# Kernel optimization log

Measured on AMD Instinct MI355X. Metric: run time of the kernel, lower is better.

The kernel has to match this reference:

```python
import jax, jax.numpy as jnp
import numpy as np
from jax import lax

N, M, T, V, C_IN, C_OUT, KT, PAD = 16, 2, 300, 25, 64, 64, 9, 4
BN_EPS = 1e-5

# NTU-RGB+D 25-joint skeleton edges (0-indexed), symmetric, plus self-loops
_NTU_EDGES = [(0,1),(1,20),(2,20),(3,2),(4,20),(5,4),(6,5),(7,6),(8,20),(9,8),
              (10,9),(11,10),(12,0),(13,12),(14,13),(15,14),(16,0),(17,16),
              (18,17),(19,18),(21,22),(22,7),(23,24),(24,11)]

def _build_adj():
    A = np.zeros((V, V), dtype=np.float32)
    for i, j in _NTU_EDGES:
        A[i, j] = 1.0
        A[j, i] = 1.0
    A += np.eye(V, dtype=np.float32)  # self-loops (DGL GCN preprocessing)
    return jnp.asarray(A)


def setup_inputs() -> dict:
    key = jax.random.key(0)
    ks = jax.random.split(key, 8)
    stdv = 1.0 / np.sqrt(C_OUT)
    # conv_init: normal(0, sqrt(2/(out_channels*prod(kernel))))
    conv_std = np.sqrt(2.0 / (C_OUT * KT * 1))
    return {
        "h": jax.random.normal(ks[0], (N * M * T * V, C_IN), dtype=jnp.float32),
        "adj": _build_adj(),
        "gcn_w": jax.random.uniform(ks[1], (C_IN, C_OUT), minval=-stdv, maxval=stdv, dtype=jnp.float32),
        "gcn_b": jax.random.uniform(ks[2], (C_OUT,), minval=-stdv, maxval=stdv, dtype=jnp.float32),
        "conv_w": conv_std * jax.random.normal(ks[3], (C_OUT, C_OUT, KT, 1), dtype=jnp.float32),
        "conv_b": jnp.zeros((C_OUT,), dtype=jnp.float32),
        "bn_gamma": jnp.ones((C_OUT,), dtype=jnp.float32),
        "bn_beta": jnp.zeros((C_OUT,), dtype=jnp.float32),
        "bn_mean": 0.1 * jax.random.normal(ks[4], (C_OUT,), dtype=jnp.float32),
        "bn_var": jax.random.uniform(ks[5], (C_OUT,), minval=0.5, maxval=1.5, dtype=jnp.float32),
    }


def reference(h, adj, gcn_w, gcn_b, conv_w, conv_b, bn_gamma, bn_beta, bn_mean, bn_var):
    # ---- GCNLayer (dropout is identity at eval) ----
    # symmetric norm = deg^{-1/2}, identical across the N*M*T copies of the skeleton
    norm = adj.sum(axis=1) ** -0.5                      # (V,)
    x = h @ gcn_w                                        # (N*M*T*V, C_OUT)
    x = x.reshape(-1, V, C_OUT) * norm[:, None]          # pre-norm scale
    x = jnp.einsum('vu,buc->bvc', adj, x)                # copy_src + sum aggregation
    x = x * norm[:, None] + gcn_b                        # post-norm scale + bias
    x = jax.nn.relu(x)

    # ---- TemporalConvNetwork ----
    v = x.reshape(N, M, T, V, C_OUT)
    v = v.transpose(0, 1, 4, 2, 3).reshape(N * M, C_OUT, T, V)   # (NM, C, T, V)
    v = lax.conv_general_dilated(v, conv_w, window_strides=(1, 1),
                                 padding=[(PAD, PAD), (0, 0)],
                                 dimension_numbers=('NCHW', 'OIHW', 'NCHW'))
    v = v + conv_b[None, :, None, None]
    inv_std = bn_gamma / jnp.sqrt(bn_var + BN_EPS)       # eval-mode BatchNorm2d
    v = (v - bn_mean[None, :, None, None]) * inv_std[None, :, None, None] + bn_beta[None, :, None, None]
    v = jax.nn.relu(v)
    v = v.reshape(N, M, C_OUT, T, V).transpose(0, 1, 3, 4, 2)    # (N, M, T, V, C)

    # ---- residual (downt is None since in_feats == out_feats and stride == 1) ----
    return v + h.reshape(N, M, T, V, C_IN)
```

## Files before the change

### kernel.cpp

```cpp
#include <hip/hip_runtime.h>
#include <hip/hip_bf16.h>


typedef __bf16 bf16x8 __attribute__((ext_vector_type(8)));
typedef __bf16 bf16x4 __attribute__((ext_vector_type(4)));
typedef float  f32x4  __attribute__((ext_vector_type(4)));

#define Y_OFF   0
#define WC2_OFF 30720000
#define WGT_OFF 30793728
#define A2P_OFF 30801920
#define SC_OFF  30803968
#define SH_OFF  30804224

__global__ __launch_bounds__(256) void prep_kernel(
    const float* __restrict__ adj, const float* __restrict__ gcn_w,
    const float* __restrict__ conv_w, const float* __restrict__ conv_b,
    const float* __restrict__ bn_g, const float* __restrict__ bn_b,
    const float* __restrict__ bn_m, const float* __restrict__ bn_v,
    __bf16* __restrict__ wc2, __bf16* __restrict__ wgt,
    __bf16* __restrict__ a2p, float* __restrict__ scale, float* __restrict__ shift) {
  int tid = threadIdx.x;
  for (int e = blockIdx.x * 256 + tid; e < 36864; e += gridDim.x * 256) {
    int j = e & 7, t1 = e >> 3, c = t1 & 63, g = t1 >> 6;
    int kap = g * 8 + j, kt = kap >> 6, ci = kap & 63;
    wc2[e] = (__bf16)conv_w[(c * 64 + ci) * 9 + kt];
  }
  if (blockIdx.x == 0) {
    for (int e = tid; e < 4096; e += 256) {
      int c = e >> 6, k = e & 63;
      wgt[e] = (__bf16)gcn_w[k * 64 + c];
    }
  } else if (blockIdx.x == 1) {
    for (int e = tid; e < 1024; e += 256) {
      int v = e >> 5, u = e & 31;
      float val = 0.f;
      if (v < 25 && u < 25) {
        float dv = 0.f, du = 0.f;
        for (int t = 0; t < 25; ++t) { dv += adj[v * 25 + t]; du += adj[u * 25 + t]; }
        val = rsqrtf(dv) * adj[v * 25 + u] * rsqrtf(du);
      }
      a2p[e] = (__bf16)val;
    }
  } else if (blockIdx.x == 2) {
    if (tid < 64) {
      float sc = bn_g[tid] * rsqrtf(bn_v[tid] + 1e-5f);
      scale[tid] = sc;
      shift[tid] = (conv_b[tid] - bn_m[tid]) * sc + bn_b[tid];
    }
  }
}

__global__ __launch_bounds__(64) void gcn_kernel(
    const float* __restrict__ h, const __bf16* __restrict__ wgt_g,
    const __bf16* __restrict__ a2p_g, const float* __restrict__ gcn_b,
    __bf16* __restrict__ y) {
  __shared__ __align__(16) __bf16 hb[2048];
  __shared__ __align__(16) __bf16 x1t[64 * 40];
  int lane = threadIdx.x;
  int l15 = lane & 15, quad = lane >> 4;
  int skel = blockIdx.x;
  int nm = skel / 300, tloc = skel - nm * 300;

  bf16x8 awg[4][2];
  for (int mt = 0; mt < 4; ++mt)
    for (int kk = 0; kk < 2; ++kk)
      awg[mt][kk] = *(const bf16x8*)&wgt_g[(mt * 16 + l15) * 64 + kk * 32 + quad * 8];
  bf16x8 ba[2];
  for (int nt = 0; nt < 2; ++nt)
    ba[nt] = *(const bf16x8*)&a2p_g[(nt * 16 + l15) * 32 + quad * 8];

  if (lane < 56) *(uint4*)&hb[1600 + lane * 8] = (uint4){0u, 0u, 0u, 0u};
  for (int it = 0; it < 7; ++it) {
    int u = it * 4 + quad;
    if (u < 25) {
      float4 hv = *(const float4*)&h[(skel * 25 + u) * 64 + l15 * 4];
      bf16x4 b4; b4[0] = (__bf16)hv.x; b4[1] = (__bf16)hv.y; b4[2] = (__bf16)hv.z; b4[3] = (__bf16)hv.w;
      int ch = l15 >> 1;
      *(bf16x4*)&hb[u * 64 + (((ch ^ (u & 7)) * 8) | ((l15 & 1) * 4))] = b4;
    }
  }
  for (int mt = 0; mt < 4; ++mt)
    for (int nt = 0; nt < 2; ++nt) {
      f32x4 acc = {0.f, 0.f, 0.f, 0.f};
      int u = nt * 16 + l15;
      for (int kk = 0; kk < 2; ++kk) {
        bf16x8 b = *(const bf16x8*)&hb[u * 64 + (((kk * 4 + quad) ^ (u & 7)) * 8)];
        acc = __builtin_amdgcn_mfma_f32_16x16x32_bf16(awg[mt][kk], b, acc, 0, 0, 0);
      }
      int c0 = mt * 16 + quad * 4;
      for (int r = 0; r < 4; ++r) x1t[(c0 + r) * 40 + u] = (__bf16)acc[r];
    }
  for (int mt = 0; mt < 4; ++mt)
    for (int nt = 0; nt < 2; ++nt) {
      f32x4 acc = {0.f, 0.f, 0.f, 0.f};
      bf16x8 a = *(const bf16x8*)&x1t[(mt * 16 + l15) * 40 + quad * 8];
      acc = __builtin_amdgcn_mfma_f32_16x16x32_bf16(a, ba[nt], acc, 0, 0, 0);
      int v = nt * 16 + l15, c0 = mt * 16 + quad * 4;
      if (v < 25) {
        float4 bias = *(const float4*)&gcn_b[c0];
        bf16x4 o;
        o[0] = (__bf16)fmaxf(acc[0] + bias.x, 0.f);
        o[1] = (__bf16)fmaxf(acc[1] + bias.y, 0.f);
        o[2] = (__bf16)fmaxf(acc[2] + bias.z, 0.f);
        o[3] = (__bf16)fmaxf(acc[3] + bias.w, 0.f);
        int ch = (c0 >> 3) ^ (v & 7);
        *(bf16x4*)&hb[v * 64 + ((ch * 8) | (c0 & 7))] = o;
      }
    }
  for (int e = lane; e < 200; e += 64) {
    int v = e >> 3, ch = e & 7;
    uint4 val = *(const uint4*)&hb[v * 64 + ((ch ^ (v & 7)) * 8)];
    *(uint4*)&y[((nm * 25 + v) * 300 + tloc) * 64 + ch * 8] = val;
  }
}

__global__ __launch_bounds__(256, 6) void conv_kernel(
    const __bf16* __restrict__ y, const __bf16* __restrict__ wc2,
    const float* __restrict__ scale, const float* __restrict__ shift,
    const float* __restrict__ h, float* __restrict__ out) {
  __shared__ __align__(16) __bf16 my[72 * 64];
  int tid = threadIdx.x, w = tid >> 6, lane = tid & 63;
  int l15 = lane & 15, quad = lane >> 4;
  int ti = blockIdx.x, vv = blockIdx.y, nm = blockIdx.z;
  int t0 = (ti < 4) ? ti * 64 : 236;

  {
    const __bf16* ybase = &y[((nm * 25 + vv) * 300) * 64];
    uint4 stg[3];
    for (int it = 0; it < 3; ++it) {
      int idx = it * 256 + tid;
      uint4 val = {0u, 0u, 0u, 0u};
      if (idx < 576) {
        int r = idx >> 3, ch = idx & 7, tg = t0 - 4 + r;
        if (tg >= 0 && tg < 300) val = *(const uint4*)&ybase[tg * 64 + ch * 8];
      }
      stg[it] = val;
    }
    for (int it = 0; it < 3; ++it) {
      int idx = it * 256 + tid;
      if (idx < 576) {
        int r = idx >> 3, ch = idx & 7;
        *(uint4*)&my[r * 64 + ((ch ^ (r & 7)) * 8)] = stg[it];
      }
    }
  }

  int c0 = w * 16 + quad * 4;
  float4 hr[4];
#pragma unroll
  for (int n = 0; n < 4; ++n) {
    int tt = t0 + n * 16 + l15;
    hr[n] = *(const float4*)&h[((nm * 300 + tt) * 25 + vv) * 64 + c0];
  }

  __syncthreads();

  f32x4 acc[4];
#pragma unroll
  for (int n = 0; n < 4; ++n) acc[n] = (f32x4){0.f, 0.f, 0.f, 0.f};

  bf16x8 a[4];
#pragma unroll
  for (int p = 0; p < 4; ++p)
    a[p] = *(const bf16x8*)&wc2[((p * 4 + quad) * 64 + w * 16 + l15) * 8];
#pragma unroll
  for (int kk = 0; kk < 18; ++kk) {
    bf16x8 areg = a[kk & 3];
    int kt = kk >> 1, chb = (kk & 1) * 4 + quad;
#pragma unroll
    for (int n = 0; n < 4; ++n) {
      int row = n * 16 + l15 + kt;
      bf16x8 b = *(const bf16x8*)&my[row * 64 + ((chb ^ (row & 7)) * 8)];
      acc[n] = __builtin_amdgcn_mfma_f32_16x16x32_bf16(areg, b, acc[n], 0, 0, 0);
    }
    if (kk + 4 < 18)
      a[kk & 3] = *(const bf16x8*)&wc2[(((kk + 4) * 4 + quad) * 64 + w * 16 + l15) * 8];
  }

  float4 sc = *(const float4*)&scale[c0];
  float4 sh = *(const float4*)&shift[c0];
#pragma unroll
  for (int n = 0; n < 4; ++n) {
    int tt = t0 + n * 16 + l15;
    int idx = ((nm * 300 + tt) * 25 + vv) * 64 + c0;
    float4 o;
    o.x = fmaxf(acc[n][0] * sc.x + sh.x, 0.f) + hr[n].x;
    o.y = fmaxf(acc[n][1] * sc.y + sh.y, 0.f) + hr[n].y;
    o.z = fmaxf(acc[n][2] * sc.z + sh.z, 0.f) + hr[n].z;
    o.w = fmaxf(acc[n][3] * sc.w + sh.w, 0.f) + hr[n].w;
    *(float4*)&out[idx] = o;
  }
}

extern "C" void kernel_launch(void* const* d_in, const int* in_sizes, int n_in,
                              void* d_out, int out_size, void* d_ws, size_t ws_size,
                              hipStream_t stream) {
  const float* h      = (const float*)d_in[0];
  const float* adj    = (const float*)d_in[1];
  const float* gcn_w  = (const float*)d_in[2];
  const float* gcn_b  = (const float*)d_in[3];
  const float* conv_w = (const float*)d_in[4];
  const float* conv_b = (const float*)d_in[5];
  const float* bn_g   = (const float*)d_in[6];
  const float* bn_b   = (const float*)d_in[7];
  const float* bn_m   = (const float*)d_in[8];
  const float* bn_v   = (const float*)d_in[9];
  float* out = (float*)d_out;
  char* ws = (char*)d_ws;

  __bf16* y_ws   = (__bf16*)(ws + Y_OFF);
  __bf16* wc2    = (__bf16*)(ws + WC2_OFF);
  __bf16* wgt    = (__bf16*)(ws + WGT_OFF);
  __bf16* a2p    = (__bf16*)(ws + A2P_OFF);
  float*  scale  = (float*)(ws + SC_OFF);
  float*  shift  = (float*)(ws + SH_OFF);

  prep_kernel<<<64, 256, 0, stream>>>(adj, gcn_w, conv_w, conv_b, bn_g, bn_b, bn_m, bn_v,
                                      wc2, wgt, a2p, scale, shift);
  gcn_kernel<<<9600, 64, 0, stream>>>(h, wgt, a2p, gcn_b, y_ws);
  conv_kernel<<<dim3(5, 25, 32), 256, 0, stream>>>(y_ws, wc2, scale, shift, h, out);
}
```

Baseline: 171.3 us.

## Switch temporal conv to 32x32x16 MFMA tiles with re-laid-out weights

Replaces the conv kernel's 16x16x32 MFMA tiling (each wave computing 16 channels × 64 time steps) with 32x32x16 MFMA (each wave computing 32 channels × 32 time steps). The conv weight pre-layout and the LDS swizzle are changed to match the new operand fragments. Weight fragments are now loaded from global memory every step instead of being rotated through registers. The intent is fewer instructions and better LDS reuse per MFMA. The trade-off is more global weight loads and a different epilogue store pattern, with channel strides of 8 between the four output groups.

Result: slower. 188.8 us (+10.3%).

```diff
diff --git a/kernel.cpp b/kernel.cpp
--- a/kernel.cpp
+++ b/kernel.cpp
@@ -5,6 +5,7 @@
 typedef __bf16 bf16x8 __attribute__((ext_vector_type(8)));
 typedef __bf16 bf16x4 __attribute__((ext_vector_type(4)));
 typedef float  f32x4  __attribute__((ext_vector_type(4)));
+typedef float  f32x16 __attribute__((ext_vector_type(16)));
 
 #define Y_OFF   0
 #define WC2_OFF 30720000
@@ -23,7 +24,8 @@
   int tid = threadIdx.x;
   for (int e = blockIdx.x * 256 + tid; e < 36864; e += gridDim.x * 256) {
     int j = e & 7, t1 = e >> 3, c = t1 & 63, g = t1 >> 6;
-    int kap = g * 8 + j, kt = kap >> 6, ci = kap & 63;
+    int kt = g >> 3, ks = (g >> 1) & 3, hi = g & 1;
+    int ci = ks * 16 + hi * 8 + j;
     wc2[e] = (__bf16)conv_w[(c * 64 + ci) * 9 + kt];
   }
   if (blockIdx.x == 0) {
@@ -121,7 +123,8 @@
     const float* __restrict__ h, float* __restrict__ out) {
   __shared__ __align__(16) __bf16 my[72 * 64];
   int tid = threadIdx.x, w = tid >> 6, lane = tid & 63;
-  int l15 = lane & 15, quad = lane >> 4;
+  int l31 = lane & 31, hi = lane >> 5;
+  int wc = w & 1, wt = w >> 1;
   int ti = blockIdx.x, vv = blockIdx.y, nm = blockIdx.z;
   int t0 = (ti < 4) ? ti * 64 : 236;
 
@@ -132,64 +135,53 @@
       int idx = it * 256 + tid;
       uint4 val = {0u, 0u, 0u, 0u};
       if (idx < 576) {
-        int r = idx >> 3, ch = idx & 7, tg = t0 - 4 + r;
-        if (tg >= 0 && tg < 300) val = *(const uint4*)&ybase[tg * 64 + ch * 8];
+        int r = idx >> 3, cc = idx & 7, tg = t0 - 4 + r;
+        if (tg >= 0 && tg < 300) val = *(const uint4*)&ybase[tg * 64 + cc * 8];
       }
       stg[it] = val;
     }
     for (int it = 0; it < 3; ++it) {
       int idx = it * 256 + tid;
       if (idx < 576) {
-        int r = idx >> 3, ch = idx & 7;
-        *(uint4*)&my[r * 64 + ((ch ^ (r & 7)) * 8)] = stg[it];
-      }
-    }
-  }
-
-  int c0 = w * 16 + quad * 4;
+        int r = idx >> 3, cc = idx & 7;
+        int pos = ((cc >> 1) | ((cc & 1) << 2)) ^ (r & 7);
+        *(uint4*)&my[r * 64 + pos * 8] = stg[it];
+      }
+    }
+  }
+
+  int cbase = wc * 32 + hi * 4;
+  int tt = t0 + wt * 32 + l31;
+  int obase = ((nm * 300 + tt) * 25 + vv) * 64 + cbase;
   float4 hr[4];
 #pragma unroll
-  for (int n = 0; n < 4; ++n) {
-    int tt = t0 + n * 16 + l15;
-    hr[n] = *(const float4*)&h[((nm * 300 + tt) * 25 + vv) * 64 + c0];
-  }
+  for (int q = 0; q < 4; ++q) hr[q] = *(const float4*)&h[obase + q * 8];
 
   __syncthreads();
 
-  f32x4 acc[4];
+  f32x16 acc = {0.f, 0.f, 0.f, 0.f, 0.f, 0.f, 0.f, 0.f,
+                0.f, 0.f, 0.f, 0.f, 0.f, 0.f, 0.f, 0.f};
+
+  const __bf16* aptr = wc2 + (hi * 64 + wc * 32 + l31) * 8;
+  int rbase = wt * 32 + l31;
 #pragma unroll
-  for (int n = 0; n < 4; ++n) acc[n] = (f32x4){0.f, 0.f, 0.f, 0.f};
-
-  bf16x8 a[4];
+  for (int s = 0; s < 36; ++s) {
+    bf16x8 a = *(const bf16x8*)(aptr + s * 1024);
+    int row = rbase + (s >> 2);
+    bf16x8 b = *(const bf16x8*)&my[row * 64 + ((((s & 3) | (hi << 2)) ^ (row & 7)) * 8)];
+    acc = __builtin_amdgcn_mfma_f32_32x32x16_bf16(a, b, acc, 0, 0, 0);
+  }
+
 #pragma unroll
-  for (int p = 0; p < 4; ++p)
-    a[p] = *(const bf16x8*)&wc2[((p * 4 + quad) * 64 + w * 16 + l15) * 8];
-#pragma unroll
-  for (int kk = 0; kk < 18; ++kk) {
-    bf16x8 areg = a[kk & 3];
-    int kt = kk >> 1, chb = (kk & 1) * 4 + quad;
-#pragma unroll
-    for (int n = 0; n < 4; ++n) {
-      int row = n * 16 + l15 + kt;
-      bf16x8 b = *(const bf16x8*)&my[row * 64 + ((chb ^ (row & 7)) * 8)];
-      acc[n] = __builtin_amdgcn_mfma_f32_16x16x32_bf16(areg, b, acc[n], 0, 0, 0);
-    }
-    if (kk + 4 < 18)
-      a[kk & 3] = *(const bf16x8*)&wc2[(((kk + 4) * 4 + quad) * 64 + w * 16 + l15) * 8];
-  }
-
-  float4 sc = *(const float4*)&scale[c0];
-  float4 sh = *(const float4*)&shift[c0];
-#pragma unroll
-  for (int n = 0; n < 4; ++n) {
-    int tt = t0 + n * 16 + l15;
-    int idx = ((nm * 300 + tt) * 25 + vv) * 64 + c0;
+  for (int q = 0; q < 4; ++q) {
+    float4 s4 = *(const float4*)&scale[cbase + q * 8];
+    float4 h4 = *(const float4*)&shift[cbase + q * 8];
     float4 o;
-    o.x = fmaxf(acc[n][0] * sc.x + sh.x, 0.f) + hr[n].x;
-    o.y = fmaxf(acc[n][1] * sc.y + sh.y, 0.f) + hr[n].y;
-    o.z = fmaxf(acc[n][2] * sc.z + sh.z, 0.f) + hr[n].z;
-    o.w = fmaxf(acc[n][3] * sc.w + sh.w, 0.f) + hr[n].w;
-    *(float4*)&out[idx] = o;
+    o.x = fmaxf(acc[q * 4 + 0] * s4.x + h4.x, 0.f) + hr[q].x;
+    o.y = fmaxf(acc[q * 4 + 1] * s4.y + h4.y, 0.f) + hr[q].y;
+    o.z = fmaxf(acc[q * 4 + 2] * s4.z + h4.z, 0.f) + hr[q].z;
+    o.w = fmaxf(acc[q * 4 + 3] * s4.w + h4.w, 0.f) + hr[q].w;
+    *(float4*)&out[obase + q * 8] = o;
   }
 }
 
```

## Split conv blocks into single-wave 32-timestep tiles covering all output channels

Applied to the files above, without the earlier changes.

The temporal conv kernel now runs one 64-thread wave per block. Each block handles 32 timesteps across all 64 output channels, instead of a 4-wave block handling 64 timesteps with 16 channels per wave. This drops the __syncthreads, cuts the LDS tile to 40 rows, and quadruples the grid, aiming for better occupancy and latency hiding. In exchange, each block re-stages a halo of 8 rows for half as many output timesteps, loads weights inside the MFMA loop without prefetch, and loads the residual in the epilogue rather than early.

Result: slower. 185.5 us (+8.3%).

```diff
diff --git a/kernel.cpp b/kernel.cpp
--- a/kernel.cpp
+++ b/kernel.cpp
@@ -115,81 +115,68 @@
   }
 }
 
-__global__ __launch_bounds__(256, 6) void conv_kernel(
+__global__ __launch_bounds__(64, 6) void conv_kernel(
     const __bf16* __restrict__ y, const __bf16* __restrict__ wc2,
     const float* __restrict__ scale, const float* __restrict__ shift,
     const float* __restrict__ h, float* __restrict__ out) {
-  __shared__ __align__(16) __bf16 my[72 * 64];
-  int tid = threadIdx.x, w = tid >> 6, lane = tid & 63;
+  __shared__ __align__(16) __bf16 my[40 * 64];
+  int lane = threadIdx.x;
   int l15 = lane & 15, quad = lane >> 4;
-  int ti = blockIdx.x, vv = blockIdx.y, nm = blockIdx.z;
-  int t0 = (ti < 4) ? ti * 64 : 236;
+  int bid = blockIdx.x;
+  int item = bid >> 1, th = bid & 1;
+  int ti = item % 5, rest = item / 5;
+  int vv = rest % 25, nm = rest / 25;
+  int t0 = ((ti < 4) ? ti * 64 : 236) + th * 32;
 
   {
     const __bf16* ybase = &y[((nm * 25 + vv) * 300) * 64];
-    uint4 stg[3];
-    for (int it = 0; it < 3; ++it) {
-      int idx = it * 256 + tid;
+#pragma unroll
+    for (int it = 0; it < 5; ++it) {
+      int idx = it * 64 + lane;
+      int r = idx >> 3, cc = idx & 7, tg = t0 - 4 + r;
       uint4 val = {0u, 0u, 0u, 0u};
-      if (idx < 576) {
-        int r = idx >> 3, ch = idx & 7, tg = t0 - 4 + r;
-        if (tg >= 0 && tg < 300) val = *(const uint4*)&ybase[tg * 64 + ch * 8];
-      }
-      stg[it] = val;
-    }
-    for (int it = 0; it < 3; ++it) {
-      int idx = it * 256 + tid;
-      if (idx < 576) {
-        int r = idx >> 3, ch = idx & 7;
-        *(uint4*)&my[r * 64 + ((ch ^ (r & 7)) * 8)] = stg[it];
-      }
-    }
-  }
-
-  int c0 = w * 16 + quad * 4;
-  float4 hr[4];
-#pragma unroll
-  for (int n = 0; n < 4; ++n) {
-    int tt = t0 + n * 16 + l15;
-    hr[n] = *(const float4*)&h[((nm * 300 + tt) * 25 + vv) * 64 + c0];
-  }
-
-  __syncthreads();
-
-  f32x4 acc[4];
-#pragma unroll
-  for (int n = 0; n < 4; ++n) acc[n] = (f32x4){0.f, 0.f, 0.f, 0.f};
-
-  bf16x8 a[4];
-#pragma unroll
-  for (int p = 0; p < 4; ++p)
-    a[p] = *(const bf16x8*)&wc2[((p * 4 + quad) * 64 + w * 16 + l15) * 8];
+      if (tg >= 0 && tg < 300) val = *(const uint4*)&ybase[tg * 64 + cc * 8];
+      *(uint4*)&my[r * 64 + ((cc ^ (r & 7)) * 8)] = val;
+    }
+  }
+
+  f32x4 acc[4][2];
+#pragma unroll
+  for (int m = 0; m < 4; ++m)
+#pragma unroll
+    for (int n = 0; n < 2; ++n) acc[m][n] = (f32x4){0.f, 0.f, 0.f, 0.f};
+
 #pragma unroll
   for (int kk = 0; kk < 18; ++kk) {
-    bf16x8 areg = a[kk & 3];
     int kt = kk >> 1, chb = (kk & 1) * 4 + quad;
-#pragma unroll
-    for (int n = 0; n < 4; ++n) {
-      int row = n * 16 + l15 + kt;
-      bf16x8 b = *(const bf16x8*)&my[row * 64 + ((chb ^ (row & 7)) * 8)];
-      acc[n] = __builtin_amdgcn_mfma_f32_16x16x32_bf16(areg, b, acc[n], 0, 0, 0);
-    }
-    if (kk + 4 < 18)
-      a[kk & 3] = *(const bf16x8*)&wc2[(((kk + 4) * 4 + quad) * 64 + w * 16 + l15) * 8];
-  }
-
-  float4 sc = *(const float4*)&scale[c0];
-  float4 sh = *(const float4*)&shift[c0];
-#pragma unroll
-  for (int n = 0; n < 4; ++n) {
-    int tt = t0 + n * 16 + l15;
-    int idx = ((nm * 300 + tt) * 25 + vv) * 64 + c0;
-    float4 o;
-    o.x = fmaxf(acc[n][0] * sc.x + sh.x, 0.f) + hr[n].x;
-    o.y = fmaxf(acc[n][1] * sc.y + sh.y, 0.f) + hr[n].y;
-    o.z = fmaxf(acc[n][2] * sc.z + sh.z, 0.f) + hr[n].z;
-    o.w = fmaxf(acc[n][3] * sc.w + sh.w, 0.f) + hr[n].w;
-    *(float4*)&out[idx] = o;
+    int r0 = l15 + kt, r1 = 16 + l15 + kt;
+    bf16x8 b0 = *(const bf16x8*)&my[r0 * 64 + ((chb ^ (r0 & 7)) * 8)];
+    bf16x8 b1 = *(const bf16x8*)&my[r1 * 64 + ((chb ^ (r1 & 7)) * 8)];
+#pragma unroll
+    for (int m = 0; m < 4; ++m) {
+      bf16x8 a = *(const bf16x8*)&wc2[((kk * 4 + quad) * 64 + m * 16 + l15) * 8];
+      acc[m][0] = __builtin_amdgcn_mfma_f32_16x16x32_bf16(a, b0, acc[m][0], 0, 0, 0);
+      acc[m][1] = __builtin_amdgcn_mfma_f32_16x16x32_bf16(a, b1, acc[m][1], 0, 0, 0);
+    }
+  }
+
+#pragma unroll
+  for (int m = 0; m < 4; ++m) {
+    int c0 = m * 16 + quad * 4;
+    float4 sc = *(const float4*)&scale[c0];
+    float4 sh = *(const float4*)&shift[c0];
+#pragma unroll
+    for (int n = 0; n < 2; ++n) {
+      int tt = t0 + n * 16 + l15;
+      int idx = ((nm * 300 + tt) * 25 + vv) * 64 + c0;
+      float4 hr = *(const float4*)&h[idx];
+      float4 o;
+      o.x = fmaxf(acc[m][n][0] * sc.x + sh.x, 0.f) + hr.x;
+      o.y = fmaxf(acc[m][n][1] * sc.y + sh.y, 0.f) + hr.y;
+      o.z = fmaxf(acc[m][n][2] * sc.z + sh.z, 0.f) + hr.z;
+      o.w = fmaxf(acc[m][n][3] * sc.w + sh.w, 0.f) + hr.w;
+      *(float4*)&out[idx] = o;
+    }
   }
 }
 
@@ -219,5 +206,5 @@
   prep_kernel<<<64, 256, 0, stream>>>(adj, gcn_w, conv_w, conv_b, bn_g, bn_b, bn_m, bn_v,
                                       wc2, wgt, a2p, scale, shift);
   gcn_kernel<<<9600, 64, 0, stream>>>(h, wgt, a2p, gcn_b, y_ws);
-  conv_kernel<<<dim3(5, 25, 32), 256, 0, stream>>>(y_ws, wc2, scale, shift, h, out);
-}
+  conv_kernel<<<8000, 64, 0, stream>>>(y_ws, wc2, scale, shift, h, out);
+}
```
